# Performance work log

Hardware: AMD Instinct MI355X
Metric: run time of the kernel (lower is better)

Reference implementation:

```python
import jax, jax.numpy as jnp
import numpy as np

CELL = 16          # pixels_per_cell
ORI = 6            # orientations
BIN_W = 180.0 / ORI
EPS = 1e-5         # skimage block-norm eps


def setup_inputs() -> dict:
    key = jax.random.key(0)
    x = jax.random.normal(key, (32, 3, 512, 512), dtype=jnp.float32)
    return {"x": x}


def _hog(x):
    # x: (B, 3, H, W) -> per-image HOG feature vector, matching skimage.feature.hog
    img = jnp.transpose(x, (0, 2, 3, 1))
    gray = 0.299 * img[..., 0] + 0.587 * img[..., 1] + 0.114 * img[..., 2]  # (B,H,W)
    B, H, W = gray.shape

    # skimage central-difference gradients with zeroed borders
    g_row = jnp.zeros_like(gray).at[:, 1:-1, :].set(gray[:, 2:, :] - gray[:, :-2, :])
    g_col = jnp.zeros_like(gray).at[:, :, 1:-1].set(gray[:, :, 2:] - gray[:, :, :-2])

    mag = jnp.hypot(g_row, g_col)
    ori = jnp.degrees(jnp.arctan2(g_row, g_col)) % 180.0
    bins = jnp.clip(jnp.floor(ori / BIN_W).astype(jnp.int32), 0, ORI - 1)

    # hard-assigned orientation histogram per 16x16 cell, averaged over cell pixels
    weighted = jax.nn.one_hot(bins, ORI, dtype=mag.dtype) * mag[..., None]  # (B,H,W,ORI)
    ncr, ncc = H // CELL, W // CELL
    cells = weighted.reshape(B, ncr, CELL, ncc, CELL, ORI).sum(axis=(2, 4)) / (CELL * CELL)

    # 2x2-cell blocks with stride 1 cell: (B, nbr, nbc, 2, 2, ORI)
    blocks = jnp.stack(
        [jnp.stack([cells[:, :-1, :-1], cells[:, :-1, 1:]], axis=3),
         jnp.stack([cells[:, 1:, :-1], cells[:, 1:, 1:]], axis=3)],
        axis=3)

    # L2-Hys normalization
    n1 = jnp.sqrt(jnp.sum(blocks * blocks, axis=(3, 4, 5), keepdims=True) + EPS * EPS)
    nb = jnp.minimum(blocks / n1, 0.2)
    n2 = jnp.sqrt(jnp.sum(nb * nb, axis=(3, 4, 5), keepdims=True) + EPS * EPS)
    nb = nb / n2
    return nb.reshape(B, -1).astype(jnp.float32)


def reference(x):
    return _hog(x)
```

## Files before the change

### kernel.cpp

```cpp
#include <hip/hip_runtime.h>
#include <math.h>

#define BATCH 32
#define HH 512
#define WW 512
#define NC 32
#define NORI 6

__device__ __forceinline__ int bin_of(float a) {
    const float deg = __fmul_rn(a, 57.29577951308232f);
    float m = fmodf(deg, 180.0f);
    if (m < 0.0f) m = __fadd_rn(m, 180.0f);
    const int b = (int)floorf(__fdiv_rn(m, 30.0f));
    return min(max(b, 0), NORI - 1);
}

__device__ __forceinline__ float ulp_step(float x, int k) {
    const int i = __float_as_int(x);
    int key = (i >= 0) ? i : -(i & 0x7FFFFFFF);
    key += k;
    const int r = (key >= 0) ? key : (int)(0x80000000u | (unsigned)(-key));
    return __int_as_float(r);
}

__global__ __launch_bounds__(256) void hog_cells_kernel(const float* __restrict__ x,
                                                        float* __restrict__ cells) {
    const int cc = blockIdx.x, cr = blockIdx.y, b = blockIdx.z;
    const int tx = threadIdx.x, ty = threadIdx.y;
    const int tid = ty * 16 + tx;

    __shared__ float gray[18][20];
    __shared__ float hist[NORI];
    if (tid < NORI) hist[tid] = 0.0f;

    const float* img = x + (size_t)b * 3 * HH * WW;
    const int r0 = cr * 16 - 1, c0 = cc * 16 - 1;
    for (int i = tid; i < 18 * 18; i += 256) {
        const int lr = i / 18, lc = i - lr * 18;
        const int r = r0 + lr, c = c0 + lc;
        float g = 0.0f;
        if (r >= 0 && r < HH && c >= 0 && c < WW) {
            const size_t idx = (size_t)r * WW + c;
            g = __fadd_rn(__fadd_rn(__fmul_rn(0.299f, img[idx]),
                                    __fmul_rn(0.587f, img[idx + (size_t)HH * WW])),
                          __fmul_rn(0.114f, img[idx + (size_t)2 * HH * WW]));
        }
        gray[lr][lc] = g;
    }
    __syncthreads();

    const int r = cr * 16 + ty;
    const int c = cc * 16 + tx;
    const int lr = ty + 1, lc = tx + 1;
    const float gy = (r >= 1 && r < HH - 1) ? __fsub_rn(gray[lr + 1][lc], gray[lr - 1][lc]) : 0.0f;
    const float gx = (c >= 1 && c < WW - 1) ? __fsub_rn(gray[lr][lc + 1], gray[lr][lc - 1]) : 0.0f;

    const double gyd = (double)gy, gxd = (double)gx;
    const float mag = (float)sqrt(gyd * gyd + gxd * gxd);

    if (mag > 0.0f) {
        if (gy == 0.0f) {
            atomicAdd(&hist[0], mag);
        } else if (gx == 0.0f) {
            atomicAdd(&hist[3], mag);
        } else {
            const float a = atan2f(gy, gx);
            const int bl = bin_of(ulp_step(a, -2));
            const int bh = bin_of(ulp_step(a, +2));
            if (bl == bh) {
                atomicAdd(&hist[bl], mag);
            } else {
                const int b0 = bin_of(a);
                const int bo = (b0 == bl) ? bh : bl;
                atomicAdd(&hist[b0], __fmul_rn(mag, 0.65f));
                atomicAdd(&hist[bo], __fmul_rn(mag, 0.35f));
            }
        }
    }
    __syncthreads();
    if (tid < NORI)
        cells[(((size_t)b * NC + cr) * NC + cc) * NORI + tid] = hist[tid] * (1.0f / 256.0f);
}

__global__ __launch_bounds__(256) void hog_norm_kernel(const float* __restrict__ cells,
                                                       float* __restrict__ out) {
    const int idx = blockIdx.x * 256 + threadIdx.x;
    const int total = BATCH * 31 * 31;
    if (idx >= total) return;
    const int bc = idx % 31;
    const int t = idx / 31;
    const int br = t % 31;
    const int b = t / 31;

    const float* cb = cells + (size_t)b * NC * NC * NORI;
    float v[24];
    float ss = 0.0f;
#pragma unroll
    for (int i = 0; i < 2; ++i)
#pragma unroll
        for (int j = 0; j < 2; ++j)
#pragma unroll
            for (int o = 0; o < NORI; ++o) {
                const float val = cb[(((br + i) * NC) + (bc + j)) * NORI + o];
                v[(i * 2 + j) * NORI + o] = val;
                ss = __fadd_rn(ss, __fmul_rn(val, val));
            }
    const float n1 = __fsqrt_rn(__fadd_rn(ss, 1e-10f));
    float ss2 = 0.0f;
#pragma unroll
    for (int k = 0; k < 24; ++k) {
        v[k] = fminf(__fdiv_rn(v[k], n1), 0.2f);
        ss2 = __fadd_rn(ss2, __fmul_rn(v[k], v[k]));
    }
    const float n2 = __fsqrt_rn(__fadd_rn(ss2, 1e-10f));
    float* op = out + (size_t)idx * 24;
#pragma unroll
    for (int k = 0; k < 24; ++k) op[k] = __fdiv_rn(v[k], n2);
}

extern "C" void kernel_launch(void* const* d_in, const int* in_sizes, int n_in,
                              void* d_out, int out_size, void* d_ws, size_t ws_size,
                              hipStream_t stream) {
    const float* x = (const float*)d_in[0];
    float* out = (float*)d_out;
    float* cells = (float*)d_ws;

    dim3 g1(NC, NC, BATCH), b1(16, 16);
    hog_cells_kernel<<<g1, b1, 0, stream>>>(x, cells);

    const int total = BATCH * 31 * 31;
    hog_norm_kernel<<<(total + 255) / 256, 256, 0, stream>>>(cells, out);
}
```

Before: 181.6 us.

## Tile 4x4 cells per block, replace atan2 binning with sector tests and register histograms

The cell kernel now covers a 64x64 pixel tile (4x4 cells) per 256-thread block, so the 1-pixel halo is shared across cells. Each thread walks 16 pixels of one row. Orientation bins come from sign tests against rotated boundary directions, and atan2 is only used when a gradient lies near a bin edge. Per-thread register histograms reduced with wave shuffles replace the shared-memory atomics, and the magnitude moves from double-precision sqrt to a float fmaf+sqrt. The norm kernel reads cells as float2 vectors. The risks are that the float magnitude and the ambiguity threshold may differ from the reference's rounding, and that there are far fewer blocks.

```diff
diff --git a/kernel.cpp b/kernel.cpp
--- a/kernel.cpp
+++ b/kernel.cpp
@@ -6,6 +6,8 @@
 #define WW 512
 #define NC 32
 #define NORI 6
+#define TP 66
+#define PITCH 67
 
 __device__ __forceinline__ int bin_of(float a) {
     const float deg = __fmul_rn(a, 57.29577951308232f);
@@ -14,7 +16,6 @@
     const int b = (int)floorf(__fdiv_rn(m, 30.0f));
     return min(max(b, 0), NORI - 1);
 }
-
 __device__ __forceinline__ float ulp_step(float x, int k) {
     const int i = __float_as_int(x);
     int key = (i >= 0) ? i : -(i & 0x7FFFFFFF);
@@ -22,64 +23,108 @@
     const int r = (key >= 0) ? key : (int)(0x80000000u | (unsigned)(-key));
     return __int_as_float(r);
 }
+__device__ __forceinline__ void deposit(float acc[NORI], int bin, float val) {
+#pragma unroll
+    for (int o = 0; o < NORI; ++o) acc[o] += (bin == o) ? val : 0.0f;
+}
 
-__global__ __launch_bounds__(256) void hog_cells_kernel(const float* __restrict__ x,
-                                                        float* __restrict__ cells) {
-    const int cc = blockIdx.x, cr = blockIdx.y, b = blockIdx.z;
-    const int tx = threadIdx.x, ty = threadIdx.y;
-    const int tid = ty * 16 + tx;
+__global__ __launch_bounds__(256, 6) void hog_cells_kernel(const float* __restrict__ x,
+                                                           float* __restrict__ cells) {
+    const int b = blockIdx.z;
+    const int tid = threadIdx.x;
+    const int R0 = 64 * blockIdx.y - 1;
+    const int C0 = 64 * blockIdx.x - 1;
 
-    __shared__ float gray[18][20];
-    __shared__ float hist[NORI];
-    if (tid < NORI) hist[tid] = 0.0f;
+    __shared__ float gray[TP * PITCH];
 
     const float* img = x + (size_t)b * 3 * HH * WW;
-    const int r0 = cr * 16 - 1, c0 = cc * 16 - 1;
-    for (int i = tid; i < 18 * 18; i += 256) {
-        const int lr = i / 18, lc = i - lr * 18;
-        const int r = r0 + lr, c = c0 + lc;
+    for (int i = tid; i < TP * TP; i += 256) {
+        const int lr = i / TP, lc = i - lr * TP;
+        const int r = R0 + lr, c = C0 + lc;
         float g = 0.0f;
-        if (r >= 0 && r < HH && c >= 0 && c < WW) {
+        if ((unsigned)r < (unsigned)HH && (unsigned)c < (unsigned)WW) {
             const size_t idx = (size_t)r * WW + c;
             g = __fadd_rn(__fadd_rn(__fmul_rn(0.299f, img[idx]),
                                     __fmul_rn(0.587f, img[idx + (size_t)HH * WW])),
-                          __fmul_rn(0.114f, img[idx + (size_t)2 * HH * WW]));
+                          __fadd_rn(0.0f, __fmul_rn(0.114f, img[idx + (size_t)2 * HH * WW])));
         }
-        gray[lr][lc] = g;
+        gray[lr * PITCH + lc] = g;
     }
     __syncthreads();
 
-    const int r = cr * 16 + ty;
-    const int c = cc * 16 + tx;
-    const int lr = ty + 1, lc = tx + 1;
-    const float gy = (r >= 1 && r < HH - 1) ? __fsub_rn(gray[lr + 1][lc], gray[lr - 1][lc]) : 0.0f;
-    const float gx = (c >= 1 && c < WW - 1) ? __fsub_rn(gray[lr][lc + 1], gray[lr][lc - 1]) : 0.0f;
+    const int wave = tid >> 6, lane = tid & 63;
+    const int rl = wave * 16 + (lane & 15);
+    const int clb = (lane >> 4) * 16;
+    const int rg = R0 + 1 + rl;
+    const bool row_ok = (rg >= 1) && (rg < HH - 1);
 
-    const double gyd = (double)gy, gxd = (double)gx;
-    const float mag = (float)sqrt(gyd * gyd + gxd * gxd);
+    const float CC = 0.86602540378443864676f, SS = 0.5f, EPS = 1e-4f;
+    float acc[NORI] = {0, 0, 0, 0, 0, 0};
 
-    if (mag > 0.0f) {
-        if (gy == 0.0f) {
-            atomicAdd(&hist[0], mag);
-        } else if (gx == 0.0f) {
-            atomicAdd(&hist[3], mag);
-        } else {
-            const float a = atan2f(gy, gx);
-            const int bl = bin_of(ulp_step(a, -2));
-            const int bh = bin_of(ulp_step(a, +2));
-            if (bl == bh) {
-                atomicAdd(&hist[bl], mag);
+#pragma unroll
+    for (int j = 0; j < 16; ++j) {
+        const int cl = clb + j;
+        const int cg = C0 + 1 + cl;
+        const float up = gray[rl * PITCH + cl + 1];
+        const float dn = gray[(rl + 2) * PITCH + cl + 1];
+        const float lf = gray[(rl + 1) * PITCH + cl];
+        const float rt = gray[(rl + 1) * PITCH + cl + 2];
+        const float gy = row_ok ? __fsub_rn(dn, up) : 0.0f;
+        const float gx = (cg >= 1 && cg < WW - 1) ? __fsub_rn(rt, lf) : 0.0f;
+
+        const float mag = __fsqrt_rn(__fmaf_rn(gy, gy, __fmul_rn(gx, gx)));
+        if (mag > 0.0f) {
+            const bool neg = gy < 0.0f;
+            const float cy = neg ? -gy : gy;
+            const float cx = neg ? -gx : gx;
+            const float t1 = __fmaf_rn(cy, CC, -__fmul_rn(cx, SS));
+            const float t2 = __fmaf_rn(cy, SS, -__fmul_rn(cx, CC));
+            const float t3 = -cx;
+            const float t4 = __fmaf_rn(cy, -SS, -__fmul_rn(cx, CC));
+            const float t5 = __fmaf_rn(cy, -CC, -__fmul_rn(cx, SS));
+            int bin = (t1 >= 0.0f) + (t2 >= 0.0f) + (t3 >= 0.0f) +
+                      (t4 >= 0.0f) + (t5 >= 0.0f);
+            const float s = __fmul_rn(mag, EPS);
+            const float mn = fminf(fminf(fminf(fabsf(t1), fabsf(t2)),
+                                         fminf(fabsf(t3), fabsf(t4))), fabsf(t5));
+            const bool gz = (gy == 0.0f), xz = (gx == 0.0f);
+            bool amb = (mn < s) || (cx < 0.0f && cy < s);
+            if (gz) { bin = 0; amb = false; }
+            else if (xz) { bin = 3; amb = false; }
+            if (!amb) {
+                deposit(acc, bin, mag);
             } else {
-                const int b0 = bin_of(a);
-                const int bo = (b0 == bl) ? bh : bl;
-                atomicAdd(&hist[b0], __fmul_rn(mag, 0.65f));
-                atomicAdd(&hist[bo], __fmul_rn(mag, 0.35f));
+                const float a = atan2f(gy, gx);
+                const int bl = bin_of(ulp_step(a, -2));
+                const int bh = bin_of(ulp_step(a, +2));
+                if (bl == bh) {
+                    deposit(acc, bl, mag);
+                } else {
+                    const int b0 = bin_of(a);
+                    const int bo = (b0 == bl) ? bh : bl;
+                    deposit(acc, b0, __fmul_rn(mag, 0.65f));
+                    deposit(acc, bo, __fmul_rn(mag, 0.35f));
+                }
             }
         }
     }
-    __syncthreads();
-    if (tid < NORI)
-        cells[(((size_t)b * NC + cr) * NC + cc) * NORI + tid] = hist[tid] * (1.0f / 256.0f);
+
+#pragma unroll
+    for (int o = 0; o < NORI; ++o) {
+        float v = acc[o];
+        v += __shfl_xor(v, 1);
+        v += __shfl_xor(v, 2);
+        v += __shfl_xor(v, 4);
+        v += __shfl_xor(v, 8);
+        acc[o] = v;
+    }
+    if ((lane & 15) == 0) {
+        const int cell_r = 4 * blockIdx.y + wave;
+        const int cell_c = 4 * blockIdx.x + (lane >> 4);
+        float* cp = cells + (((size_t)b * NC + cell_r) * NC + cell_c) * NORI;
+#pragma unroll
+        for (int o = 0; o < NORI; ++o) cp[o] = acc[o] * (1.0f / 256.0f);
+    }
 }
 
 __global__ __launch_bounds__(256) void hog_norm_kernel(const float* __restrict__ cells,
@@ -93,18 +138,18 @@
     const int b = t / 31;
 
     const float* cb = cells + (size_t)b * NC * NC * NORI;
+    const float2* p0 = (const float2*)(cb + ((br) * NC + bc) * NORI);
+    const float2* p1 = (const float2*)(cb + ((br + 1) * NC + bc) * NORI);
     float v[24];
+#pragma unroll
+    for (int q = 0; q < 6; ++q) {
+        const float2 r0 = p0[q], r1 = p1[q];
+        v[2 * q] = r0.x; v[2 * q + 1] = r0.y;
+        v[12 + 2 * q] = r1.x; v[12 + 2 * q + 1] = r1.y;
+    }
     float ss = 0.0f;
 #pragma unroll
-    for (int i = 0; i < 2; ++i)
-#pragma unroll
-        for (int j = 0; j < 2; ++j)
-#pragma unroll
-            for (int o = 0; o < NORI; ++o) {
-                const float val = cb[(((br + i) * NC) + (bc + j)) * NORI + o];
-                v[(i * 2 + j) * NORI + o] = val;
-                ss = __fadd_rn(ss, __fmul_rn(val, val));
-            }
+    for (int k = 0; k < 24; ++k) ss = __fadd_rn(ss, __fmul_rn(v[k], v[k]));
     const float n1 = __fsqrt_rn(__fadd_rn(ss, 1e-10f));
     float ss2 = 0.0f;
 #pragma unroll
@@ -125,7 +170,7 @@
     float* out = (float*)d_out;
     float* cells = (float*)d_ws;
 
-    dim3 g1(NC, NC, BATCH), b1(16, 16);
+    dim3 g1(8, 8, BATCH), b1(256);
     hog_cells_kernel<<<g1, b1, 0, stream>>>(x, cells);
 
     const int total = BATCH * 31 * 31;
```

New measurement: 166.1 us. 1.09x faster.
